# Kernel optimization log

Hardware: AMD Instinct MI355X
Metric: run time of the kernel (lower is better)

The kernel has to match this reference:

```python
import jax, jax.numpy as jnp
import numpy as np

RES = 128
SH_DIM = 9            # (deg+1)^2, deg=2
CH = SH_DIM * 3 + 1   # 28: 3*9 SH rgb coeffs + 1 sigma
AABB_MIN = -1.0
AABB_MAX = 1.0
STEP = (AABB_MAX - AABB_MIN) / (RES - 1)   # voxel_len = mean(aabb_size/(res-1))
UNIFORM = 0.5
N_SAMPLES = int(RES * 3 / UNIFORM)         # plenoxels count: 768
EPS = 1e-10


def sh_encode_deg2(d):
    # real spherical harmonics basis, degree 2 (9 coefficients), on normalized dirs
    d = d / jnp.linalg.norm(d, axis=-1, keepdims=True)
    x, y, z = d[..., 0], d[..., 1], d[..., 2]
    C0 = 0.28209479177387814
    C1 = 0.4886025119029199
    C20, C21, C22 = 1.0925484305920792, -1.0925484305920792, 0.31539156525252005
    C23, C24 = -1.0925484305920792, 0.5462742152960396
    return jnp.stack([
        jnp.full_like(x, C0),
        -C1 * y, C1 * z, -C1 * x,
        C20 * x * y, C21 * y * z, C22 * (2.0 * z * z - x * x - y * y),
        C23 * x * z, C24 * (x * x - y * y),
    ], axis=-1)


def grid_sample_3d(grid, pts):
    # grid: [D,H,W,C]; pts: [...,3] in [-1,1], (x,y,z) with x->W, y->H, z->D.
    # Matches torch F.grid_sample(mode='bilinear', padding_mode='zeros', align_corners=True).
    D, H, W, C = grid.shape
    lead = pts.shape[:-1]
    p = pts.reshape(-1, 3)
    x = (p[:, 0] + 1.0) * 0.5 * (W - 1)
    y = (p[:, 1] + 1.0) * 0.5 * (H - 1)
    z = (p[:, 2] + 1.0) * 0.5 * (D - 1)
    x0f, y0f, z0f = jnp.floor(x), jnp.floor(y), jnp.floor(z)
    fx, fy, fz = x - x0f, y - y0f, z - z0f
    x0 = x0f.astype(jnp.int32)
    y0 = y0f.astype(jnp.int32)
    z0 = z0f.astype(jnp.int32)
    flat = grid.reshape(-1, C)
    out = jnp.zeros((p.shape[0], C), grid.dtype)
    for dz in (0, 1):
        for dy in (0, 1):
            for dx in (0, 1):
                xi, yi, zi = x0 + dx, y0 + dy, z0 + dz
                valid = (xi >= 0) & (xi < W) & (yi >= 0) & (yi < H) & (zi >= 0) & (zi < D)
                w = ((fx if dx else 1.0 - fx)
                     * (fy if dy else 1.0 - fy)
                     * (fz if dz else 1.0 - fz)) * valid
                idx = (jnp.clip(zi, 0, D - 1) * H + jnp.clip(yi, 0, H - 1)) * W + jnp.clip(xi, 0, W - 1)
                out = out + w[:, None] * flat[idx]
    return out.reshape(lead + (C,))


def setup_inputs() -> dict:
    key = jax.random.key(0)
    k1, k2, k3 = jax.random.split(key, 3)
    B = 4096
    # origins on a radius-3 sphere, aimed at jittered targets inside the unit box
    o = jax.random.normal(k1, (B, 3), dtype=jnp.float32)
    rays_o = 3.0 * o / jnp.linalg.norm(o, axis=-1, keepdims=True)
    tgt = jax.random.uniform(k2, (B, 3), dtype=jnp.float32, minval=-0.5, maxval=0.5)
    d = tgt - rays_o
    rays_d = d / jnp.linalg.norm(d, axis=-1, keepdims=True)
    grid_data = 0.1 * jax.random.normal(k3, (RES ** 3, CH), dtype=jnp.float32)
    grid_data = grid_data.at[:, -1].add(0.1)  # ini_sigma offset
    return {"rays_d": rays_d, "rays_o": rays_o, "grid_data": grid_data}


def reference(rays_d, rays_o, grid_data):
    B = rays_d.shape[0]
    aabb_lo = jnp.full((3,), AABB_MIN, rays_o.dtype)
    aabb_hi = jnp.full((3,), AABB_MAX, rays_o.dtype)
    # ray-AABB intersection (no_grad in torch)
    t_pos = (aabb_hi - rays_o) / rays_d
    t_neg = (aabb_lo - rays_o) / rays_d
    t_in = jnp.minimum(t_pos, t_neg)
    t_out = jnp.maximum(t_pos, t_neg)
    start = jnp.max(t_in, axis=-1)                  # [B]
    stop = jnp.min(t_out, axis=-1, keepdims=True)   # [B,1]
    # tensor_linspace from start+u*step to start+u*step*n, then clamp max=stop
    w = jnp.linspace(0.0, 1.0, N_SAMPLES, dtype=rays_o.dtype)  # [S]
    s0 = start + UNIFORM * STEP
    s1 = start + UNIFORM * STEP * N_SAMPLES
    intersections = s0[:, None] * (1.0 - w) + s1[:, None] * w   # [B,S]
    intersections = jnp.minimum(intersections, stop)
    t = intersections[:, :-1]                                    # [B,S-1]
    pts = rays_o[:, None, :] + t[:, :, None] * rays_d[:, None, :]
    pts = (pts - AABB_MIN) * (2.0 / (AABB_MAX - AABB_MIN)) - 1.0  # normalize to [-1,1]
    # trilinear sample of the voxel grid (torch layout: D=res0,H=res1,W=res2; x->W)
    interp = grid_sample_3d(grid_data.reshape(RES, RES, RES, CH), pts)  # [B,S-1,CH]
    sigma = interp[..., -1]
    rgb_sh = interp[..., :-1].reshape(B, N_SAMPLES - 1, 3, SH_DIM)
    sh = sh_encode_deg2(rays_d)                                   # [B,9]
    rgb = jnp.einsum('bsck,bk->bsc', rgb_sh, sh)
    # volumetric rendering
    dists = jnp.diff(intersections, axis=1) * jnp.linalg.norm(rays_d, axis=-1, keepdims=True)
    alpha = 1.0 - jnp.exp(-jax.nn.relu(sigma) * dists)
    cum_light = jnp.concatenate(
        [jnp.ones((B, 1), alpha.dtype), jnp.cumprod(1.0 - alpha[:, :-1] + EPS, axis=-1)], axis=-1)
    abs_light = alpha * cum_light
    acc_map = abs_light.sum(-1)
    rgb_map = (abs_light[..., None] * jax.nn.sigmoid(rgb)).sum(-2)
    depth = (abs_light * t).sum(-1)
    rgb_map = rgb_map + (1.0 - acc_map[:, None])  # white background
    return rgb_map, alpha, depth
```

## Files before the change

### kernel.cpp

```cpp
#include <hip/hip_runtime.h>
#include <math.h>

#define RESG 128
#define CHG 28
#define NT 767

__global__ __launch_bounds__(256) void nerf_grid_kernel(
    const float* __restrict__ rays_d,
    const float* __restrict__ rays_o,
    const float* __restrict__ grid,
    float* __restrict__ out_rgb,
    float* __restrict__ out_alpha,
    float* __restrict__ out_depth)
{
    const int ray  = blockIdx.x;
    const int tid  = threadIdx.x;
    const int lane = tid & 63;
    const int wave = tid >> 6;

    const float EPSC   = 1e-10f;
    const float INV127 = 1.0f / 127.0f;

    __shared__ float a_lds[NT + 1];
    __shared__ float r_lds[NT + 1];
    __shared__ float g_lds[NT + 1];
    __shared__ float b_lds[NT + 1];
    __shared__ float wprod[4];
    __shared__ float red[4][5];

    const float ox = rays_o[ray*3+0], oy = rays_o[ray*3+1], oz = rays_o[ray*3+2];
    const float dx = rays_d[ray*3+0], dy = rays_d[ray*3+1], dz = rays_d[ray*3+2];
    const float dnorm = sqrtf(dx*dx + dy*dy + dz*dz);

    float txp = (1.0f - ox)/dx, txn = (-1.0f - ox)/dx;
    float typ = (1.0f - oy)/dy, tyn = (-1.0f - oy)/dy;
    float tzp = (1.0f - oz)/dz, tzn = (-1.0f - oz)/dz;
    const float start = fmaxf(fmaxf(fminf(txp,txn), fminf(typ,tyn)), fminf(tzp,tzn));
    const float stop  = fminf(fminf(fmaxf(txp,txn), fmaxf(typ,tyn)), fmaxf(tzp,tzn));

    int n_proc = (int)((stop - start) * 127.0f) + 2;
    n_proc = n_proc < 0 ? 0 : (n_proc > NT ? NT : n_proc);

    const float inv = 1.0f/dnorm;
    const float nx = dx*inv, ny = dy*inv, nz = dz*inv;
    float sh0, sh1, sh2, sh3, sh4, sh5, sh6, sh7, sh8;
    {
        const float C0 = 0.28209479177387814f;
        const float C1 = 0.4886025119029199f;
        const float C20 = 1.0925484305920792f, C21 = -1.0925484305920792f;
        const float C22 = 0.31539156525252005f;
        const float C23 = -1.0925484305920792f, C24 = 0.5462742152960396f;
        sh0 = C0;
        sh1 = -C1*ny;
        sh2 =  C1*nz;
        sh3 = -C1*nx;
        sh4 = C20*nx*ny;
        sh5 = C21*ny*nz;
        sh6 = C22*(2.0f*nz*nz - nx*nx - ny*ny);
        sh7 = C23*nx*nz;
        sh8 = C24*(nx*nx - ny*ny);
    }

    const int samp   = lane >> 3;
    const int corner = lane & 7;
    const int cdx = corner & 1, cdy = (corner >> 1) & 1, cdz = corner >> 2;

    for (int base = wave*8; base < n_proc; base += 32) {
        const int s = base + samp;
        float rr = 0.0f, gg = 0.0f, bb = 0.0f, sg = 0.0f;
        float t0 = 0.0f, dist = 0.0f;
        bool live = false;
        if (s < n_proc) {
            t0 = fminf(start + (float)(s+1)*INV127, stop);
            const float t1 = fminf(start + (float)(s+2)*INV127, stop);
            dist = (t1 - t0) * dnorm;
            live = dist > 0.0f;
        }
        if (live) {
            const float gx = (ox + t0*dx + 1.0f)*63.5f;
            const float gy = (oy + t0*dy + 1.0f)*63.5f;
            const float gz = (oz + t0*dz + 1.0f)*63.5f;
            const float fx0 = floorf(gx), fy0 = floorf(gy), fz0 = floorf(gz);
            const float fx = gx - fx0, fy = gy - fy0, fz = gz - fz0;
            const int xi = (int)fx0 + cdx;
            const int yi = (int)fy0 + cdy;
            const int zi = (int)fz0 + cdz;
            const bool valid = ((unsigned)xi < (unsigned)RESG) &
                               ((unsigned)yi < (unsigned)RESG) &
                               ((unsigned)zi < (unsigned)RESG);
            const float w = (cdx ? fx : 1.0f-fx) *
                            (cdy ? fy : 1.0f-fy) *
                            (cdz ? fz : 1.0f-fz);
            if (valid && w != 0.0f) {
                const float4* row = (const float4*)(grid + (size_t)(((zi*RESG) + yi)*RESG + xi)*CHG);
                const float4 v0 = row[0], v1 = row[1], v2 = row[2], v3 = row[3];
                const float4 v4 = row[4], v5 = row[5], v6 = row[6];
                rr = w*(v0.x*sh0 + v0.y*sh1 + v0.z*sh2 + v0.w*sh3 +
                        v1.x*sh4 + v1.y*sh5 + v1.z*sh6 + v1.w*sh7 + v2.x*sh8);
                gg = w*(v2.y*sh0 + v2.z*sh1 + v2.w*sh2 + v3.x*sh3 +
                        v3.y*sh4 + v3.z*sh5 + v3.w*sh6 + v4.x*sh7 + v4.y*sh8);
                bb = w*(v4.z*sh0 + v4.w*sh1 + v5.x*sh2 + v5.y*sh3 +
                        v5.z*sh4 + v5.w*sh5 + v6.x*sh6 + v6.y*sh7 + v6.z*sh8);
                sg = w*v6.w;
            }
        }
        #pragma unroll
        for (int off = 1; off < 8; off <<= 1) {
            rr += __shfl_xor(rr, off, 64);
            gg += __shfl_xor(gg, off, 64);
            bb += __shfl_xor(bb, off, 64);
            sg += __shfl_xor(sg, off, 64);
        }
        if (corner == 0 && s < n_proc) {
            const float a = live ? 1.0f - expf(-fmaxf(sg, 0.0f)*dist) : 0.0f;
            a_lds[s] = a;
            r_lds[s] = 1.0f/(1.0f + expf(-rr));
            g_lds[s] = 1.0f/(1.0f + expf(-gg));
            b_lds[s] = 1.0f/(1.0f + expf(-bb));
        }
    }
    __syncthreads();

    for (int s = tid; s < NT; s += 256)
        out_alpha[(size_t)ray*NT + s] = (s < n_proc) ? a_lds[s] : 0.0f;

    float a_r[3], q_r[3], t_r[3], rr_r[3], gg_r[3], bb_r[3];
    #pragma unroll
    for (int k = 0; k < 3; ++k) {
        const int s = tid*3 + k;
        float a = 0.0f, rr = 0.0f, gg = 0.0f, bb = 0.0f, tt = 0.0f;
        if (s < NT) {
            tt = fminf(start + (float)(s+1)*INV127, stop);
            if (s < n_proc) {
                a  = a_lds[s];
                rr = r_lds[s]; gg = g_lds[s]; bb = b_lds[s];
            }
        }
        a_r[k] = a; q_r[k] = (s < NT) ? (1.0f - a + EPSC) : 1.0f;
        t_r[k] = tt; rr_r[k] = rr; gg_r[k] = gg; bb_r[k] = bb;
    }

    const float P = q_r[0]*q_r[1]*q_r[2];
    float incl = P;
    #pragma unroll
    for (int off = 1; off < 64; off <<= 1) {
        const float n = __shfl_up(incl, off, 64);
        if (lane >= off) incl *= n;
    }
    float excl = __shfl_up(incl, 1, 64);
    if (lane == 0) excl = 1.0f;

    if (lane == 63) wprod[wave] = incl;
    __syncthreads();
    float wpre = 1.0f;
    for (int w2 = 0; w2 < 4; ++w2) if (w2 < wave) wpre *= wprod[w2];

    float cum = wpre * excl;
    float accA = 0.0f, accR = 0.0f, accG = 0.0f, accB = 0.0f, accD = 0.0f;
    #pragma unroll
    for (int k = 0; k < 3; ++k) {
        const float abs_l = a_r[k] * cum;
        accA += abs_l;
        accR += abs_l * rr_r[k];
        accG += abs_l * gg_r[k];
        accB += abs_l * bb_r[k];
        accD += abs_l * t_r[k];
        cum *= q_r[k];
    }

    #pragma unroll
    for (int off = 32; off > 0; off >>= 1) {
        accA += __shfl_down(accA, off, 64);
        accR += __shfl_down(accR, off, 64);
        accG += __shfl_down(accG, off, 64);
        accB += __shfl_down(accB, off, 64);
        accD += __shfl_down(accD, off, 64);
    }
    if (lane == 0) {
        red[wave][0] = accA; red[wave][1] = accR; red[wave][2] = accG;
        red[wave][3] = accB; red[wave][4] = accD;
    }
    __syncthreads();
    if (tid == 0) {
        float A = 0.0f, R = 0.0f, G = 0.0f, Bv = 0.0f, D = 0.0f;
        #pragma unroll
        for (int w2 = 0; w2 < 4; ++w2) {
            A += red[w2][0]; R += red[w2][1]; G += red[w2][2];
            Bv += red[w2][3]; D += red[w2][4];
        }
        const float bg = 1.0f - A;
        out_rgb[ray*3+0] = R  + bg;
        out_rgb[ray*3+1] = G  + bg;
        out_rgb[ray*3+2] = Bv + bg;
        out_depth[ray] = D;
    }
}

extern "C" void kernel_launch(void* const* d_in, const int* in_sizes, int n_in,
                              void* d_out, int out_size, void* d_ws, size_t ws_size,
                              hipStream_t stream) {
    const float* rays_d = (const float*)d_in[0];
    const float* rays_o = (const float*)d_in[1];
    const float* grid   = (const float*)d_in[2];
    const int B = in_sizes[0] / 3;

    float* out       = (float*)d_out;
    float* out_rgb   = out;
    float* out_alpha = out + (size_t)B*3;
    float* out_depth = out + (size_t)B*3 + (size_t)B*NT;

    nerf_grid_kernel<<<B, 256, 0, stream>>>(rays_d, rays_o, grid,
                                            out_rgb, out_alpha, out_depth);
}
```

Measured before the change: 85.96 us.

## Reorder rays by direction bucket to improve grid cache locality

Adds a single-block pre-pass that buckets rays by cube-map face and an 8x8 direction cell, then builds a permutation. The main kernel processes rays in that order so that blocks running at the same time sample nearby voxels and share L2/MALL hits. The cost is an extra serial launch: one 1024-thread block with shared atomics and a single-thread prefix scan. The shared key buffer is fixed at 4096 entries, which caps B.

```diff
diff --git a/kernel.cpp b/kernel.cpp
--- a/kernel.cpp
+++ b/kernel.cpp
@@ -4,16 +4,55 @@
 #define RESG 128
 #define CHG 28
 #define NT 767
+#define NBKT 384
+
+__global__ __launch_bounds__(1024) void prep_sort(
+    const float* __restrict__ rays_d, int* __restrict__ perm, int B)
+{
+    __shared__ int cnt[NBKT];
+    __shared__ int off[NBKT];
+    __shared__ unsigned short keys[4096];
+    const int tid = threadIdx.x;
+    for (int i = tid; i < NBKT; i += 1024) cnt[i] = 0;
+    __syncthreads();
+    for (int r = tid; r < B; r += 1024) {
+        float ddx = rays_d[r*3+0], ddy = rays_d[r*3+1], ddz = rays_d[r*3+2];
+        float ax = fabsf(ddx), ay = fabsf(ddy), az = fabsf(ddz);
+        int face; float u, v, m;
+        if (ax >= ay && ax >= az) { face = (ddx < 0.f) ? 0 : 1; m = ax; u = ddy; v = ddz; }
+        else if (ay >= az)        { face = (ddy < 0.f) ? 2 : 3; m = ay; u = ddx; v = ddz; }
+        else                      { face = (ddz < 0.f) ? 4 : 5; m = az; u = ddx; v = ddy; }
+        float iu = u / m * 0.5f + 0.5f;
+        float iv = v / m * 0.5f + 0.5f;
+        int qu = min(7, max(0, (int)(iu * 8.0f)));
+        int qv = min(7, max(0, (int)(iv * 8.0f)));
+        int k = face * 64 + qu * 8 + qv;
+        keys[r] = (unsigned short)k;
+        atomicAdd(&cnt[k], 1);
+    }
+    __syncthreads();
+    if (tid == 0) {
+        int a = 0;
+        for (int i = 0; i < NBKT; ++i) { off[i] = a; a += cnt[i]; }
+    }
+    __syncthreads();
+    for (int r = tid; r < B; r += 1024) {
+        int k = keys[r];
+        int slot = atomicAdd(&off[k], 1);
+        perm[slot] = r;
+    }
+}
 
 __global__ __launch_bounds__(256) void nerf_grid_kernel(
     const float* __restrict__ rays_d,
     const float* __restrict__ rays_o,
     const float* __restrict__ grid,
+    const int*   __restrict__ perm,
     float* __restrict__ out_rgb,
     float* __restrict__ out_alpha,
     float* __restrict__ out_depth)
 {
-    const int ray  = blockIdx.x;
+    const int ray  = perm[blockIdx.x];
     const int tid  = threadIdx.x;
     const int lane = tid & 63;
     const int wave = tid >> 6;
@@ -50,15 +89,10 @@
         const float C20 = 1.0925484305920792f, C21 = -1.0925484305920792f;
         const float C22 = 0.31539156525252005f;
         const float C23 = -1.0925484305920792f, C24 = 0.5462742152960396f;
-        sh0 = C0;
-        sh1 = -C1*ny;
-        sh2 =  C1*nz;
-        sh3 = -C1*nx;
-        sh4 = C20*nx*ny;
-        sh5 = C21*ny*nz;
+        sh0 = C0;   sh1 = -C1*ny; sh2 = C1*nz; sh3 = -C1*nx;
+        sh4 = C20*nx*ny; sh5 = C21*ny*nz;
         sh6 = C22*(2.0f*nz*nz - nx*nx - ny*ny);
-        sh7 = C23*nx*nz;
-        sh8 = C24*(nx*nx - ny*ny);
+        sh7 = C23*nx*nz; sh8 = C24*(nx*nx - ny*ny);
     }
 
     const int samp   = lane >> 3;
@@ -105,15 +139,14 @@
             }
         }
         #pragma unroll
-        for (int off = 1; off < 8; off <<= 1) {
-            rr += __shfl_xor(rr, off, 64);
-            gg += __shfl_xor(gg, off, 64);
-            bb += __shfl_xor(bb, off, 64);
-            sg += __shfl_xor(sg, off, 64);
+        for (int off2 = 1; off2 < 8; off2 <<= 1) {
+            rr += __shfl_xor(rr, off2, 64);
+            gg += __shfl_xor(gg, off2, 64);
+            bb += __shfl_xor(bb, off2, 64);
+            sg += __shfl_xor(sg, off2, 64);
         }
         if (corner == 0 && s < n_proc) {
-            const float a = live ? 1.0f - expf(-fmaxf(sg, 0.0f)*dist) : 0.0f;
-            a_lds[s] = a;
+            a_lds[s] = live ? 1.0f - expf(-fmaxf(sg, 0.0f)*dist) : 0.0f;
             r_lds[s] = 1.0f/(1.0f + expf(-rr));
             g_lds[s] = 1.0f/(1.0f + expf(-gg));
             b_lds[s] = 1.0f/(1.0f + expf(-bb));
@@ -132,7 +165,7 @@
         if (s < NT) {
             tt = fminf(start + (float)(s+1)*INV127, stop);
             if (s < n_proc) {
-                a  = a_lds[s];
+                a = a_lds[s];
                 rr = r_lds[s]; gg = g_lds[s]; bb = b_lds[s];
             }
         }
@@ -143,9 +176,9 @@
     const float P = q_r[0]*q_r[1]*q_r[2];
     float incl = P;
     #pragma unroll
-    for (int off = 1; off < 64; off <<= 1) {
-        const float n = __shfl_up(incl, off, 64);
-        if (lane >= off) incl *= n;
+    for (int off2 = 1; off2 < 64; off2 <<= 1) {
+        const float n = __shfl_up(incl, off2, 64);
+        if (lane >= off2) incl *= n;
     }
     float excl = __shfl_up(incl, 1, 64);
     if (lane == 0) excl = 1.0f;
@@ -169,12 +202,12 @@
     }
 
     #pragma unroll
-    for (int off = 32; off > 0; off >>= 1) {
-        accA += __shfl_down(accA, off, 64);
-        accR += __shfl_down(accR, off, 64);
-        accG += __shfl_down(accG, off, 64);
-        accB += __shfl_down(accB, off, 64);
-        accD += __shfl_down(accD, off, 64);
+    for (int off2 = 32; off2 > 0; off2 >>= 1) {
+        accA += __shfl_down(accA, off2, 64);
+        accR += __shfl_down(accR, off2, 64);
+        accG += __shfl_down(accG, off2, 64);
+        accB += __shfl_down(accB, off2, 64);
+        accD += __shfl_down(accD, off2, 64);
     }
     if (lane == 0) {
         red[wave][0] = accA; red[wave][1] = accR; red[wave][2] = accG;
@@ -209,6 +242,9 @@
     float* out_alpha = out + (size_t)B*3;
     float* out_depth = out + (size_t)B*3 + (size_t)B*NT;
 
-    nerf_grid_kernel<<<B, 256, 0, stream>>>(rays_d, rays_o, grid,
+    int* perm = (int*)d_ws;
+
+    prep_sort<<<1, 1024, 0, stream>>>(rays_d, perm, B);
+    nerf_grid_kernel<<<B, 256, 0, stream>>>(rays_d, rays_o, grid, perm,
                                             out_rgb, out_alpha, out_depth);
 }
```

New measurement: 89.35 us. 3.9% more time.
